# Optimization experiments

Measured on AMD Instinct MI355X. Metric: run time of the kernel, lower is better.

Reference implementation:

```python
import jax, jax.numpy as jnp
import numpy as np

N_NODES = 50000
N_EDGES = 800000
IN_CH = 512
HID = 128
OUT_CH = 2
N_GRAPHS = 64
EPS = 1e-5


def _gcn_conv(x, src, dst, W, b):
    # GCNConv: out = D^-1/2 (A + I) D^-1/2 (x W) + b  (PyG semantics, self-loops added)
    n = x.shape[0]
    h = x @ W  # [N, H]
    loop = jnp.arange(n)
    src2 = jnp.concatenate([src, loop])
    dst2 = jnp.concatenate([dst, loop])
    deg = jax.ops.segment_sum(jnp.ones_like(dst2, dtype=h.dtype), dst2, num_segments=n)
    dinv = jax.lax.rsqrt(deg)  # deg >= 1 due to self-loops
    norm = dinv[src2] * dinv[dst2]  # [E+N]
    msg = h[src2] * norm[:, None]  # gather + normalize
    out = jax.ops.segment_sum(msg, dst2, num_segments=n)  # scatter-add
    return out + b


def _batchnorm_eval(x, gamma, beta, rm, rv):
    return (x - rm) * jax.lax.rsqrt(rv + EPS) * gamma + beta


def setup_inputs() -> dict:
    key = jax.random.key(0)
    ks = jax.random.split(key, 16)
    x = jax.random.normal(ks[0], (N_NODES, IN_CH), dtype=jnp.float32)
    edge_index = jax.random.randint(ks[1], (2, N_EDGES), 0, N_NODES, dtype=jnp.int64)
    batch = jnp.sort(jax.random.randint(ks[2], (N_NODES,), 0, N_GRAPHS, dtype=jnp.int64))
    s1 = 1.0 / np.sqrt(IN_CH)
    s2 = 1.0 / np.sqrt(HID)
    return {
        'x': x,
        'edge_index': edge_index,
        'batch': batch,
        'W1': jax.random.normal(ks[3], (IN_CH, HID), dtype=jnp.float32) * s1,
        'b1': jnp.zeros((HID,), dtype=jnp.float32),
        'gamma1': jax.random.normal(ks[4], (HID,), dtype=jnp.float32) * 0.1 + 1.0,
        'beta1': jax.random.normal(ks[5], (HID,), dtype=jnp.float32) * 0.1,
        'rm1': jax.random.normal(ks[6], (HID,), dtype=jnp.float32) * 0.1,
        'rv1': jax.random.uniform(ks[7], (HID,), dtype=jnp.float32, minval=0.5, maxval=1.5),
        'W2': jax.random.normal(ks[8], (HID, HID), dtype=jnp.float32) * s2,
        'b2': jnp.zeros((HID,), dtype=jnp.float32),
        'gamma2': jax.random.normal(ks[9], (HID,), dtype=jnp.float32) * 0.1 + 1.0,
        'beta2': jax.random.normal(ks[10], (HID,), dtype=jnp.float32) * 0.1,
        'rm2': jax.random.normal(ks[11], (HID,), dtype=jnp.float32) * 0.1,
        'rv2': jax.random.uniform(ks[12], (HID,), dtype=jnp.float32, minval=0.5, maxval=1.5),
        'Wl': jax.random.normal(ks[13], (HID, OUT_CH), dtype=jnp.float32) * s2,
        'bl': jnp.zeros((OUT_CH,), dtype=jnp.float32),
    }


def reference(x, edge_index, batch, W1, b1, gamma1, beta1, rm1, rv1,
              W2, b2, gamma2, beta2, rm2, rv2, Wl, bl):
    # Eval mode: BatchNorm uses running stats; dropout is identity.
    src, dst = edge_index[0], edge_index[1]
    h = _gcn_conv(x, src, dst, W1, b1)
    h = jax.nn.relu(_batchnorm_eval(h, gamma1, beta1, rm1, rv1))
    h = _gcn_conv(h, src, dst, W2, b2)
    h = jax.nn.relu(_batchnorm_eval(h, gamma2, beta2, rm2, rv2))
    # global mean pool over graphs in the batch
    sums = jax.ops.segment_sum(h, batch, num_segments=N_GRAPHS)  # [G, H]
    counts = jax.ops.segment_sum(jnp.ones((h.shape[0],), dtype=h.dtype), batch, num_segments=N_GRAPHS)
    pooled = sums / jnp.maximum(counts, 1.0)[:, None]
    return pooled @ Wl + bl  # [G, OUT_CH]
```

## Files before the change

### kernel.cpp

```cpp
#include <hip/hip_runtime.h>

#define EPSV 1e-5f

typedef __attribute__((ext_vector_type(8))) short short8;
typedef __attribute__((ext_vector_type(4))) float f32x4;
typedef unsigned int uint;
typedef unsigned short ushort;

__global__ __launch_bounds__(256) void init_k(int* __restrict__ cnt,
                                              const int* __restrict__ batch,
                                              int* __restrict__ gstart,
                                              int nnodes, int ngraphs) {
    int i = blockIdx.x * 256 + threadIdx.x;
    if (i < nnodes) cnt[i] = 0;
    if (blockIdx.x == 0 && threadIdx.x <= ngraphs) {
        int g = threadIdx.x;
        int lo = 0, hi = nnodes;
        while (lo < hi) {
            int mid = (lo + hi) >> 1;
            if (batch[mid] < g) lo = mid + 1; else hi = mid;
        }
        gstart[g] = lo;
    }
}

__global__ __launch_bounds__(256) void degcount_k(const int* __restrict__ dst,
                                                  int* __restrict__ cnt,
                                                  int nedges) {
    int i = blockIdx.x * 256 + threadIdx.x;
    if (i < nedges) atomicAdd(&cnt[dst[i]], 1);
}

__global__ __launch_bounds__(256) void scan1_k(const int* __restrict__ cnt,
                                               int* __restrict__ rowptr,
                                               int* __restrict__ bsum,
                                               float* __restrict__ dinv, int n) {
    __shared__ int sh[256];
    const int tx = threadIdx.x;
    const int base = blockIdx.x * 1024;
    int v[4];
    int s = 0;
#pragma unroll
    for (int j = 0; j < 4; j++) {
        int idx = base + tx * 4 + j;
        v[j] = (idx < n) ? cnt[idx] : 0;
        if (idx < n) dinv[idx] = rsqrtf(1.0f + (float)v[j]);
        s += v[j];
    }
    sh[tx] = s;
    __syncthreads();
#pragma unroll
    for (int off = 1; off < 256; off <<= 1) {
        int t = (tx >= off) ? sh[tx - off] : 0;
        __syncthreads();
        sh[tx] += t;
        __syncthreads();
    }
    int run = sh[tx] - s;
#pragma unroll
    for (int j = 0; j < 4; j++) {
        int idx = base + tx * 4 + j;
        if (idx < n) rowptr[idx] = run;
        run += v[j];
    }
    if (tx == 255) bsum[blockIdx.x] = sh[255];
}

__global__ __launch_bounds__(64) void scan2_k(int* __restrict__ bsum, int nb) {
    __shared__ int sh[64];
    const int tx = threadIdx.x;
    int v = (tx < nb) ? bsum[tx] : 0;
    sh[tx] = v;
    __syncthreads();
#pragma unroll
    for (int off = 1; off < 64; off <<= 1) {
        int t = (tx >= off) ? sh[tx - off] : 0;
        __syncthreads();
        sh[tx] += t;
        __syncthreads();
    }
    if (tx < nb) bsum[tx] = sh[tx] - v;
}

__global__ __launch_bounds__(256) void scan3_k(int* __restrict__ rowptr,
                                               int* __restrict__ cur,
                                               const int* __restrict__ bsum,
                                               int n, int nedges) {
    const int tx = threadIdx.x;
    const int base = blockIdx.x * 1024;
    int off = bsum[blockIdx.x];
#pragma unroll
    for (int j = 0; j < 4; j++) {
        int idx = base + tx * 4 + j;
        if (idx < n) {
            int r = rowptr[idx] + off;
            rowptr[idx] = r;
            cur[idx] = r;
        }
    }
    if (blockIdx.x == 0 && tx == 0) rowptr[n] = nedges;
}

__global__ __launch_bounds__(256) void fill_k(const int* __restrict__ src,
                                              const int* __restrict__ dst,
                                              int* __restrict__ cur,
                                              int* __restrict__ esrc, int nedges) {
    int i = blockIdx.x * 256 + threadIdx.x;
    if (i >= nedges) return;
    int pos = atomicAdd(&cur[dst[i]], 1);
    esrc[pos] = src[i];
}

__global__ __launch_bounds__(256) void wprep_k(const float* __restrict__ W1,
                                               const float* __restrict__ W2,
                                               ushort* __restrict__ wt1,
                                               ushort* __restrict__ wt2) {
    int i = blockIdx.x * 256 + threadIdx.x;
    if (i < 512 * 128) {
        int k = i >> 7, c = i & 127;
        unsigned u = __builtin_bit_cast(unsigned, W1[i]);
        wt1[c * 512 + k] = (ushort)((u + 0x7fffu + ((u >> 16) & 1u)) >> 16);
    } else if (i < 512 * 128 + 128 * 128) {
        int j = i - 512 * 128;
        int k = j >> 7, c = j & 127;
        unsigned u = __builtin_bit_cast(unsigned, W2[j]);
        wt2[c * 128 + k] = (ushort)((u + 0x7fffu + ((u >> 16) & 1u)) >> 16);
    }
}

template <int K>
__global__ __launch_bounds__(256) void gemm_mfma_k(const float* __restrict__ X,
                                                   const ushort* __restrict__ wT,
                                                   const float* __restrict__ dinv,
                                                   float* __restrict__ H,
                                                   ushort* __restrict__ hb16,
                                                   int nrows) {
    __shared__ ushort bsm[2][8192];

    const int tx = threadIdx.x;
    const int wu = __builtin_amdgcn_readfirstlane(tx >> 6);
    const int l = tx & 63;
    const int lrow = l & 15;
    const int kgrp = l >> 4;
    const int wrow = wu >> 1;
    const int wcol = wu & 1;
    const int row0 = blockIdx.x * 32 + wrow * 16;

    const ushort* sp[4];
#pragma unroll
    for (int q = 0; q < 4; q++) {
        int chunk = (wu * 4 + q) * 64 + l;
        int c = chunk >> 3;
        int s = (chunk & 7) ^ (c & 7);
        sp[q] = wT + (size_t)c * K + s * 8;
    }

    int arow = row0 + lrow;
    if (arow >= nrows) arow = nrows - 1;
    const float* xrow = X + (size_t)arow * K + kgrp * 8;

    f32x4 acc[4];
#pragma unroll
    for (int g = 0; g < 4; g++) acc[g] = (f32x4){0.f, 0.f, 0.f, 0.f};

    auto STAGE = [&](int buf, int k0) {
#pragma unroll
        for (int q = 0; q < 4; q++) {
            const ushort* src = sp[q] + k0;
            ushort* dst = &bsm[buf][(wu * 4 + q) * 512];
            __builtin_amdgcn_global_load_lds(
                (const __attribute__((address_space(1))) unsigned int*)(const void*)src,
                (__attribute__((address_space(3))) unsigned int*)(void*)dst,
                16, 0, 0);
        }
    };

    constexpr int NIT = K / 64;

    STAGE(0, 0);
    asm volatile("" ::: "memory");
    f32x4 c0 = *reinterpret_cast<const f32x4*>(xrow);
    f32x4 c1 = *reinterpret_cast<const f32x4*>(xrow + 4);
    f32x4 c2 = *reinterpret_cast<const f32x4*>(xrow + 32);
    f32x4 c3 = *reinterpret_cast<const f32x4*>(xrow + 36);
    f32x4 d0 = c0, d1 = c1, d2 = c2, d3 = c3;
    if (NIT > 1) {
        d0 = *reinterpret_cast<const f32x4*>(xrow + 64);
        d1 = *reinterpret_cast<const f32x4*>(xrow + 68);
        d2 = *reinterpret_cast<const f32x4*>(xrow + 96);
        d3 = *reinterpret_cast<const f32x4*>(xrow + 100);
    }

#pragma unroll
    for (int i = 0; i < NIT; i++) {
        if (i == 0 && NIT > 1)   asm volatile("s_waitcnt vmcnt(8)" ::: "memory");
        else if (i + 1 < NIT)    asm volatile("s_waitcnt vmcnt(4)" ::: "memory");
        else                     asm volatile("s_waitcnt vmcnt(0)" ::: "memory");
        __builtin_amdgcn_s_barrier();
        __builtin_amdgcn_sched_barrier(0);

        if (i + 1 < NIT) STAGE((i + 1) & 1, (i + 1) * 64);
        asm volatile("" ::: "memory");

        f32x4 e0 = d0, e1 = d1, e2 = d2, e3 = d3;
        if (i + 2 < NIT) {
            const float* nx = xrow + (i + 2) * 64;
            e0 = *reinterpret_cast<const f32x4*>(nx);
            e1 = *reinterpret_cast<const f32x4*>(nx + 4);
            e2 = *reinterpret_cast<const f32x4*>(nx + 32);
            e3 = *reinterpret_cast<const f32x4*>(nx + 36);
        }

        const ushort* b = bsm[i & 1];
#pragma unroll
        for (int sub = 0; sub < 2; sub++) {
            short8 ah, al;
#pragma unroll
            for (int j = 0; j < 8; j++) {
                float f = (sub == 0) ? ((j < 4) ? c0[j] : c1[j - 4])
                                     : ((j < 4) ? c2[j] : c3[j - 4]);
                unsigned u = __builtin_bit_cast(unsigned, f);
                ah[j] = (short)(u >> 16);
                float hif = __builtin_bit_cast(float, u & 0xffff0000u);
                float lof = f - hif;
                al[j] = (short)(__builtin_bit_cast(unsigned, lof) >> 16);
            }
#pragma unroll
            for (int g = 0; g < 4; g++) {
                int cc = (wcol * 4 + g) * 16 + lrow;
                int phys = (sub * 4 + kgrp) ^ (cc & 7);
                short8 bb = *reinterpret_cast<const short8*>(&b[cc * 64 + phys * 8]);
                acc[g] = __builtin_amdgcn_mfma_f32_16x16x32_bf16(ah, bb, acc[g], 0, 0, 0);
                acc[g] = __builtin_amdgcn_mfma_f32_16x16x32_bf16(al, bb, acc[g], 0, 0, 0);
            }
        }

        c0 = d0; c1 = d1; c2 = d2; c3 = d3;
        d0 = e0; d1 = e1; d2 = e2; d3 = e3;
    }

#pragma unroll
    for (int r = 0; r < 4; r++) {
        int row = row0 + kgrp * 4 + r;
        if (row < nrows) {
            float dn = dinv[row];
            float* hrow = H + (size_t)row * 128 + wcol * 64 + lrow;
            ushort* hbrow = hb16 + (size_t)row * 128 + wcol * 64 + lrow;
#pragma unroll
            for (int g = 0; g < 4; g++) {
                float v = acc[g][r];
                hrow[g * 16] = v;
                unsigned u = __builtin_bit_cast(unsigned, v * dn);
                hbrow[g * 16] = (ushort)((u + 0x7fffu + ((u >> 16) & 1u)) >> 16);
            }
        }
    }
}

__global__ __launch_bounds__(256) void agg_k(const float* __restrict__ H,
                                             const uint* __restrict__ hb,
                                             const int* __restrict__ rowptr,
                                             const int* __restrict__ esrc,
                                             const float* __restrict__ dinv,
                                             const float* __restrict__ bias,
                                             const float* __restrict__ gamma,
                                             const float* __restrict__ beta,
                                             const float* __restrict__ rm,
                                             const float* __restrict__ rv,
                                             float* __restrict__ OUT,
                                             int nnodes) {
    int node = blockIdx.x * 4 + (threadIdx.x >> 6);
    if (node >= nnodes) return;
    node = __builtin_amdgcn_readfirstlane(node);
    const int l = threadIdx.x & 63;
    const int c = l * 2;
    const float dn = dinv[node];
    const int beg = rowptr[node], end = rowptr[node + 1];

    float2 hv = *reinterpret_cast<const float2*>(H + (size_t)node * 128 + c);
    float ax0 = hv.x * dn, ay0 = hv.y * dn;
    float ax1 = 0.f, ay1 = 0.f, ax2 = 0.f, ay2 = 0.f, ax3 = 0.f, ay3 = 0.f;
    const uint* hbl = hb + l;

    int j = beg;
    for (; j + 3 < end; j += 4) {
        int s0 = esrc[j], s1 = esrc[j + 1], s2 = esrc[j + 2], s3 = esrc[j + 3];
        uint u0 = hbl[(size_t)s0 * 64];
        uint u1 = hbl[(size_t)s1 * 64];
        uint u2 = hbl[(size_t)s2 * 64];
        uint u3 = hbl[(size_t)s3 * 64];
        ax0 += __builtin_bit_cast(float, u0 << 16);
        ay0 += __builtin_bit_cast(float, u0 & 0xffff0000u);
        ax1 += __builtin_bit_cast(float, u1 << 16);
        ay1 += __builtin_bit_cast(float, u1 & 0xffff0000u);
        ax2 += __builtin_bit_cast(float, u2 << 16);
        ay2 += __builtin_bit_cast(float, u2 & 0xffff0000u);
        ax3 += __builtin_bit_cast(float, u3 << 16);
        ay3 += __builtin_bit_cast(float, u3 & 0xffff0000u);
    }
    for (; j < end; j++) {
        uint u0 = hbl[(size_t)esrc[j] * 64];
        ax0 += __builtin_bit_cast(float, u0 << 16);
        ay0 += __builtin_bit_cast(float, u0 & 0xffff0000u);
    }
    float accx = (ax0 + ax1) + (ax2 + ax3);
    float accy = (ay0 + ay1) + (ay2 + ay3);

    float v0 = accx * dn + bias[c];
    float v1 = accy * dn + bias[c + 1];
    v0 = (v0 - rm[c])     * rsqrtf(rv[c] + EPSV)     * gamma[c]     + beta[c];
    v1 = (v1 - rm[c + 1]) * rsqrtf(rv[c + 1] + EPSV) * gamma[c + 1] + beta[c + 1];
    v0 = fmaxf(v0, 0.0f);
    v1 = fmaxf(v1, 0.0f);

    *reinterpret_cast<float2*>(OUT + (size_t)node * 128 + c) = make_float2(v0, v1);
}

__global__ __launch_bounds__(256) void pool1_k(const float* __restrict__ V,
                                               const int* __restrict__ gstart,
                                               float* __restrict__ partial) {
    __shared__ float sh[256];
    const int g = blockIdx.x >> 5;
    const int p = blockIdx.x & 31;
    const int tx = threadIdx.x;
    const int ch = tx & 127;
    const int sub = tx >> 7;
    const int beg = gstart[g], end = gstart[g + 1];
    const int chunk = (end - beg + 31) >> 5;
    const int s = beg + p * chunk;
    const int e = min(s + chunk, end);
    float acc = 0.0f;
    for (int i = s + sub; i < e; i += 2)
        acc += V[(size_t)i * 128 + ch];
    sh[tx] = acc;
    __syncthreads();
    if (tx < 128)
        partial[(size_t)blockIdx.x * 128 + tx] = sh[tx] + sh[tx + 128];
}

__global__ __launch_bounds__(128) void pool2_k(const float* __restrict__ partial,
                                               const int* __restrict__ gstart,
                                               float* __restrict__ pooled) {
    const int g = blockIdx.x;
    const int ch = threadIdx.x;
    float s = 0.0f;
#pragma unroll
    for (int p = 0; p < 32; p++)
        s += partial[(size_t)((g << 5) + p) * 128 + ch];
    float cnt = fmaxf((float)(gstart[g + 1] - gstart[g]), 1.0f);
    pooled[g * 128 + ch] = s / cnt;
}

__global__ __launch_bounds__(128) void final_k(const float* __restrict__ pooled,
                                               const float* __restrict__ Wl,
                                               const float* __restrict__ bl,
                                               float* __restrict__ out) {
    int tx = threadIdx.x;
    int g = tx >> 1, o = tx & 1;
    float s = 0.0f;
#pragma unroll 8
    for (int c = 0; c < 128; c++) s += pooled[g * 128 + c] * Wl[c * 2 + o];
    out[tx] = s + bl[o];
}

extern "C" void kernel_launch(void* const* d_in, const int* in_sizes, int n_in,
                              void* d_out, int out_size, void* d_ws, size_t ws_size,
                              hipStream_t stream) {
    const float* x      = (const float*)d_in[0];
    const int*   ei     = (const int*)d_in[1];
    const int*   batch  = (const int*)d_in[2];
    const float* W1     = (const float*)d_in[3];
    const float* b1     = (const float*)d_in[4];
    const float* gamma1 = (const float*)d_in[5];
    const float* beta1  = (const float*)d_in[6];
    const float* rm1    = (const float*)d_in[7];
    const float* rv1    = (const float*)d_in[8];
    const float* W2     = (const float*)d_in[9];
    const float* b2     = (const float*)d_in[10];
    const float* gamma2 = (const float*)d_in[11];
    const float* beta2  = (const float*)d_in[12];
    const float* rm2    = (const float*)d_in[13];
    const float* rv2    = (const float*)d_in[14];
    const float* Wl     = (const float*)d_in[15];
    const float* bl     = (const float*)d_in[16];
    float* out = (float*)d_out;

    const int nnodes  = in_sizes[2];
    const int nedges  = in_sizes[1] / 2;
    const int ngraphs = 64;
    const int* srcp = ei;
    const int* dstp = ei + nedges;

    float* wsA     = (float*)d_ws;
    float* wsB     = wsA + (size_t)nnodes * 128;
    float* dinv    = wsB + (size_t)nnodes * 128;
    float* pooled  = dinv + nnodes;
    float* partial = pooled + 64 * 128;
    int*   cnt     = (int*)(partial + 64 * 32 * 128);
    int*   rowptr  = cnt + nnodes;
    int*   cur     = rowptr + nnodes + 1;
    int*   bsum    = cur + nnodes;
    int*   gstart  = bsum + 64;
    int*   esrc    = gstart + 65;
    uintptr_t wp   = ((uintptr_t)(esrc + nedges) + 15) & ~(uintptr_t)15;
    ushort* wt1  = (ushort*)wp;
    ushort* wt2  = wt1 + 512 * 128;
    ushort* hb16 = wt2 + 128 * 128;
    uint*   hb   = (uint*)hb16;

    dim3 blk(256);
    const int gNodes = (nnodes + 255) / 256;
    const int gEdges = (nedges + 255) / 256;
    const int gGemm  = (nnodes + 31) / 32;
    const int gAgg   = (nnodes + 3) / 4;
    const int nScanB = (nnodes + 1023) / 1024;

    init_k<<<gNodes, blk, 0, stream>>>(cnt, batch, gstart, nnodes, ngraphs);
    wprep_k<<<(512 * 128 + 128 * 128 + 255) / 256, blk, 0, stream>>>(W1, W2, wt1, wt2);
    degcount_k<<<gEdges, blk, 0, stream>>>(dstp, cnt, nedges);
    scan1_k<<<nScanB, blk, 0, stream>>>(cnt, rowptr, bsum, dinv, nnodes);
    scan2_k<<<1, 64, 0, stream>>>(bsum, nScanB);
    scan3_k<<<nScanB, blk, 0, stream>>>(rowptr, cur, bsum, nnodes, nedges);
    fill_k<<<gEdges, blk, 0, stream>>>(srcp, dstp, cur, esrc, nedges);

    gemm_mfma_k<512><<<gGemm, blk, 0, stream>>>(x, wt1, dinv, wsA, hb16, nnodes);
    agg_k<<<gAgg, blk, 0, stream>>>(wsA, hb, rowptr, esrc, dinv, b1, gamma1, beta1,
                                    rm1, rv1, wsB, nnodes);

    gemm_mfma_k<128><<<gGemm, blk, 0, stream>>>(wsB, wt2, dinv, wsA, hb16, nnodes);
    agg_k<<<gAgg, blk, 0, stream>>>(wsA, hb, rowptr, esrc, dinv, b2, gamma2, beta2,
                                    rm2, rv2, wsB, nnodes);

    pool1_k<<<ngraphs * 32, blk, 0, stream>>>(wsB, gstart, partial);
    pool2_k<<<ngraphs, 128, 0, stream>>>(partial, gstart, pooled);
    final_k<<<1, 128, 0, stream>>>(pooled, Wl, bl, out);
}
```

Before: 263.8 us.

## Stage full weight matrix in LDS once per block and double rows per block

The GEMM kernel now loads the entire transposed bf16 weight matrix into shared memory once at block start, instead of double-buffering 64-wide K slices with per-iteration barriers and waitcnts. Blocks grow to 512 threads covering 64 rows, which halves the grid and the total weight traffic from L2. In exchange, shared-memory use reaches 128KB for K=512, limiting each CU to roughly one block. The weight load also no longer overlaps with the MFMA work.

```diff
diff --git a/kernel.cpp b/kernel.cpp
--- a/kernel.cpp
+++ b/kernel.cpp
@@ -129,13 +129,13 @@
 }
 
 template <int K>
-__global__ __launch_bounds__(256) void gemm_mfma_k(const float* __restrict__ X,
+__global__ __launch_bounds__(512) void gemm_mfma_k(const float* __restrict__ X,
                                                    const ushort* __restrict__ wT,
                                                    const float* __restrict__ dinv,
                                                    float* __restrict__ H,
                                                    ushort* __restrict__ hb16,
                                                    int nrows) {
-    __shared__ ushort bsm[2][8192];
+    __shared__ ushort wsm[128 * K];
 
     const int tx = threadIdx.x;
     const int wu = __builtin_amdgcn_readfirstlane(tx >> 6);
@@ -144,15 +144,21 @@
     const int kgrp = l >> 4;
     const int wrow = wu >> 1;
     const int wcol = wu & 1;
-    const int row0 = blockIdx.x * 32 + wrow * 16;
-
-    const ushort* sp[4];
-#pragma unroll
-    for (int q = 0; q < 4; q++) {
-        int chunk = (wu * 4 + q) * 64 + l;
-        int c = chunk >> 3;
-        int s = (chunk & 7) ^ (c & 7);
-        sp[q] = wT + (size_t)c * K + s * 8;
+    const int row0 = blockIdx.x * 64 + wrow * 16;
+
+    constexpr int NPW = K / 32;
+#pragma unroll
+    for (int q = 0; q < NPW; q++) {
+        int j = wu * NPW + q;
+        int byte0 = j * 1024 + l * 16;
+        int c = byte0 / (K * 2);
+        int slot = (byte0 % (K * 2)) >> 4;
+        const ushort* src = wT + (size_t)c * K + ((slot ^ (c & 7)) * 8);
+        ushort* dst = &wsm[j * 512];
+        __builtin_amdgcn_global_load_lds(
+            (const __attribute__((address_space(1))) unsigned int*)(const void*)src,
+            (__attribute__((address_space(3))) unsigned int*)(void*)dst,
+            16, 0, 0);
     }
 
     int arow = row0 + lrow;
@@ -163,22 +169,8 @@
 #pragma unroll
     for (int g = 0; g < 4; g++) acc[g] = (f32x4){0.f, 0.f, 0.f, 0.f};
 
-    auto STAGE = [&](int buf, int k0) {
-#pragma unroll
-        for (int q = 0; q < 4; q++) {
-            const ushort* src = sp[q] + k0;
-            ushort* dst = &bsm[buf][(wu * 4 + q) * 512];
-            __builtin_amdgcn_global_load_lds(
-                (const __attribute__((address_space(1))) unsigned int*)(const void*)src,
-                (__attribute__((address_space(3))) unsigned int*)(void*)dst,
-                16, 0, 0);
-        }
-    };
-
     constexpr int NIT = K / 64;
 
-    STAGE(0, 0);
-    asm volatile("" ::: "memory");
     f32x4 c0 = *reinterpret_cast<const f32x4*>(xrow);
     f32x4 c1 = *reinterpret_cast<const f32x4*>(xrow + 4);
     f32x4 c2 = *reinterpret_cast<const f32x4*>(xrow + 32);
@@ -191,17 +183,10 @@
         d3 = *reinterpret_cast<const f32x4*>(xrow + 100);
     }
 
+    __syncthreads();
+
 #pragma unroll
     for (int i = 0; i < NIT; i++) {
-        if (i == 0 && NIT > 1)   asm volatile("s_waitcnt vmcnt(8)" ::: "memory");
-        else if (i + 1 < NIT)    asm volatile("s_waitcnt vmcnt(4)" ::: "memory");
-        else                     asm volatile("s_waitcnt vmcnt(0)" ::: "memory");
-        __builtin_amdgcn_s_barrier();
-        __builtin_amdgcn_sched_barrier(0);
-
-        if (i + 1 < NIT) STAGE((i + 1) & 1, (i + 1) * 64);
-        asm volatile("" ::: "memory");
-
         f32x4 e0 = d0, e1 = d1, e2 = d2, e3 = d3;
         if (i + 2 < NIT) {
             const float* nx = xrow + (i + 2) * 64;
@@ -211,7 +196,6 @@
             e3 = *reinterpret_cast<const f32x4*>(nx + 36);
         }
 
-        const ushort* b = bsm[i & 1];
 #pragma unroll
         for (int sub = 0; sub < 2; sub++) {
             short8 ah, al;
@@ -225,11 +209,13 @@
                 float lof = f - hif;
                 al[j] = (short)(__builtin_bit_cast(unsigned, lof) >> 16);
             }
+            int slot = i * 8 + sub * 4 + kgrp;
 #pragma unroll
             for (int g = 0; g < 4; g++) {
                 int cc = (wcol * 4 + g) * 16 + lrow;
-                int phys = (sub * 4 + kgrp) ^ (cc & 7);
-                short8 bb = *reinterpret_cast<const short8*>(&b[cc * 64 + phys * 8]);
+                int phys = slot ^ (cc & 7);
+                short8 bb = *reinterpret_cast<const short8*>(
+                    &wsm[(size_t)cc * K + phys * 8]);
                 acc[g] = __builtin_amdgcn_mfma_f32_16x16x32_bf16(ah, bb, acc[g], 0, 0, 0);
                 acc[g] = __builtin_amdgcn_mfma_f32_16x16x32_bf16(al, bb, acc[g], 0, 0, 0);
             }
@@ -411,7 +397,7 @@
     dim3 blk(256);
     const int gNodes = (nnodes + 255) / 256;
     const int gEdges = (nedges + 255) / 256;
-    const int gGemm  = (nnodes + 31) / 32;
+    const int gGemm  = (nnodes + 63) / 64;
     const int gAgg   = (nnodes + 3) / 4;
     const int nScanB = (nnodes + 1023) / 1024;
 
@@ -423,11 +409,11 @@
     scan3_k<<<nScanB, blk, 0, stream>>>(rowptr, cur, bsum, nnodes, nedges);
     fill_k<<<gEdges, blk, 0, stream>>>(srcp, dstp, cur, esrc, nedges);
 
-    gemm_mfma_k<512><<<gGemm, blk, 0, stream>>>(x, wt1, dinv, wsA, hb16, nnodes);
+    gemm_mfma_k<512><<<gGemm, dim3(512), 0, stream>>>(x, wt1, dinv, wsA, hb16, nnodes);
     agg_k<<<gAgg, blk, 0, stream>>>(wsA, hb, rowptr, esrc, dinv, b1, gamma1, beta1,
                                     rm1, rv1, wsB, nnodes);
 
-    gemm_mfma_k<128><<<gGemm, blk, 0, stream>>>(wsB, wt2, dinv, wsA, hb16, nnodes);
+    gemm_mfma_k<128><<<gGemm, dim3(512), 0, stream>>>(wsB, wt2, dinv, wsA, hb16, nnodes);
     agg_k<<<gAgg, blk, 0, stream>>>(wsA, hb, rowptr, esrc, dinv, b2, gamma2, beta2,
                                     rm2, rv2, wsB, nnodes);
 
```

Measured after the change: 275.6 us. 1.04x slower.

## Stage X tiles through LDS and widen GEMM tile to 64 rows by 128 columns

Applied to the files above, without the earlier changes.

The GEMM now loads X tiles asynchronously into swizzled LDS with global_load_lds instead of prefetching them into registers. Each wave computes a 16x128 output strip (8 accumulators) instead of 16x64, so a block covers 64 rows and W is reused across twice as many rows. The aim is to halve the number of times W tiles are reloaded and to stream the fp32 activations more efficiently. In exchange, LDS use grows to about 64KB per block, which can limit occupancy, and the loop now waits with vmcnt(0) each iteration, dropping the finer-grained prefetch overlap.

```diff
diff --git a/kernel.cpp b/kernel.cpp
--- a/kernel.cpp
+++ b/kernel.cpp
@@ -135,90 +135,76 @@
                                                    float* __restrict__ H,
                                                    ushort* __restrict__ hb16,
                                                    int nrows) {
-    __shared__ ushort bsm[2][8192];
+    __shared__ float  lAs[2][64 * 64];
+    __shared__ ushort lBs[2][128 * 64];
 
     const int tx = threadIdx.x;
     const int wu = __builtin_amdgcn_readfirstlane(tx >> 6);
     const int l = tx & 63;
     const int lrow = l & 15;
     const int kgrp = l >> 4;
-    const int wrow = wu >> 1;
-    const int wcol = wu & 1;
-    const int row0 = blockIdx.x * 32 + wrow * 16;
-
-    const ushort* sp[4];
-#pragma unroll
-    for (int q = 0; q < 4; q++) {
-        int chunk = (wu * 4 + q) * 64 + l;
-        int c = chunk >> 3;
-        int s = (chunk & 7) ^ (c & 7);
-        sp[q] = wT + (size_t)c * K + s * 8;
-    }
-
-    int arow = row0 + lrow;
-    if (arow >= nrows) arow = nrows - 1;
-    const float* xrow = X + (size_t)arow * K + kgrp * 8;
-
-    f32x4 acc[4];
-#pragma unroll
-    for (int g = 0; g < 4; g++) acc[g] = (f32x4){0.f, 0.f, 0.f, 0.f};
+    const int rowB = blockIdx.x * 64;
+    const int row0 = rowB + wu * 16;
+
+    f32x4 acc[8];
+#pragma unroll
+    for (int g = 0; g < 8; g++) acc[g] = (f32x4){0.f, 0.f, 0.f, 0.f};
 
     auto STAGE = [&](int buf, int k0) {
 #pragma unroll
         for (int q = 0; q < 4; q++) {
-            const ushort* src = sp[q] + k0;
-            ushort* dst = &bsm[buf][(wu * 4 + q) * 512];
+            int j = wu * 4 + q;
+            int row = j * 4 + (l >> 4);
+            int slot = l & 15;
+            int grow = rowB + row;
+            if (grow >= nrows) grow = nrows - 1;
+            const float* src = X + (size_t)grow * K + k0 + ((slot ^ (row & 15)) * 4);
+            float* dst = &lAs[buf][j * 256];
             __builtin_amdgcn_global_load_lds(
                 (const __attribute__((address_space(1))) unsigned int*)(const void*)src,
                 (__attribute__((address_space(3))) unsigned int*)(void*)dst,
                 16, 0, 0);
         }
+#pragma unroll
+        for (int q = 0; q < 4; q++) {
+            int j = wu * 4 + q;
+            int col = j * 8 + (l >> 3);
+            int slot = l & 7;
+            const ushort* src = wT + (size_t)col * K + k0 + ((slot ^ (col & 7)) * 8);
+            ushort* dst = &lBs[buf][j * 512];
+            __builtin_amdgcn_global_load_lds(
+                (const __attribute__((address_space(1))) unsigned int*)(const void*)src,
+                (__attribute__((address_space(3))) unsigned int*)(void*)dst,
+                16, 0, 0);
+        }
     };
 
     constexpr int NIT = K / 64;
 
     STAGE(0, 0);
-    asm volatile("" ::: "memory");
-    f32x4 c0 = *reinterpret_cast<const f32x4*>(xrow);
-    f32x4 c1 = *reinterpret_cast<const f32x4*>(xrow + 4);
-    f32x4 c2 = *reinterpret_cast<const f32x4*>(xrow + 32);
-    f32x4 c3 = *reinterpret_cast<const f32x4*>(xrow + 36);
-    f32x4 d0 = c0, d1 = c1, d2 = c2, d3 = c3;
-    if (NIT > 1) {
-        d0 = *reinterpret_cast<const f32x4*>(xrow + 64);
-        d1 = *reinterpret_cast<const f32x4*>(xrow + 68);
-        d2 = *reinterpret_cast<const f32x4*>(xrow + 96);
-        d3 = *reinterpret_cast<const f32x4*>(xrow + 100);
-    }
 
 #pragma unroll
     for (int i = 0; i < NIT; i++) {
-        if (i == 0 && NIT > 1)   asm volatile("s_waitcnt vmcnt(8)" ::: "memory");
-        else if (i + 1 < NIT)    asm volatile("s_waitcnt vmcnt(4)" ::: "memory");
-        else                     asm volatile("s_waitcnt vmcnt(0)" ::: "memory");
+        asm volatile("s_waitcnt vmcnt(0)" ::: "memory");
         __builtin_amdgcn_s_barrier();
         __builtin_amdgcn_sched_barrier(0);
 
         if (i + 1 < NIT) STAGE((i + 1) & 1, (i + 1) * 64);
         asm volatile("" ::: "memory");
 
-        f32x4 e0 = d0, e1 = d1, e2 = d2, e3 = d3;
-        if (i + 2 < NIT) {
-            const float* nx = xrow + (i + 2) * 64;
-            e0 = *reinterpret_cast<const f32x4*>(nx);
-            e1 = *reinterpret_cast<const f32x4*>(nx + 4);
-            e2 = *reinterpret_cast<const f32x4*>(nx + 32);
-            e3 = *reinterpret_cast<const f32x4*>(nx + 36);
-        }
-
-        const ushort* b = bsm[i & 1];
-#pragma unroll
-        for (int sub = 0; sub < 2; sub++) {
+        const int buf = i & 1;
+        const int trow = wu * 16 + lrow;
+#pragma unroll
+        for (int ks = 0; ks < 2; ks++) {
+            int s16 = (ks * 4 + kgrp) * 2;
+            f32x4 a0 = *reinterpret_cast<const f32x4*>(
+                &lAs[buf][trow * 64 + ((s16 ^ lrow) & 15) * 4]);
+            f32x4 a1 = *reinterpret_cast<const f32x4*>(
+                &lAs[buf][trow * 64 + (((s16 + 1) ^ lrow) & 15) * 4]);
             short8 ah, al;
 #pragma unroll
             for (int j = 0; j < 8; j++) {
-                float f = (sub == 0) ? ((j < 4) ? c0[j] : c1[j - 4])
-                                     : ((j < 4) ? c2[j] : c3[j - 4]);
+                float f = (j < 4) ? a0[j] : a1[j - 4];
                 unsigned u = __builtin_bit_cast(unsigned, f);
                 ah[j] = (short)(u >> 16);
                 float hif = __builtin_bit_cast(float, u & 0xffff0000u);
@@ -226,17 +212,15 @@
                 al[j] = (short)(__builtin_bit_cast(unsigned, lof) >> 16);
             }
 #pragma unroll
-            for (int g = 0; g < 4; g++) {
-                int cc = (wcol * 4 + g) * 16 + lrow;
-                int phys = (sub * 4 + kgrp) ^ (cc & 7);
-                short8 bb = *reinterpret_cast<const short8*>(&b[cc * 64 + phys * 8]);
+            for (int g = 0; g < 8; g++) {
+                int cc = g * 16 + lrow;
+                int phys = (ks * 4 + kgrp) ^ (cc & 7);
+                short8 bb = *reinterpret_cast<const short8*>(
+                    &lBs[buf][cc * 64 + phys * 8]);
                 acc[g] = __builtin_amdgcn_mfma_f32_16x16x32_bf16(ah, bb, acc[g], 0, 0, 0);
                 acc[g] = __builtin_amdgcn_mfma_f32_16x16x32_bf16(al, bb, acc[g], 0, 0, 0);
             }
         }
-
-        c0 = d0; c1 = d1; c2 = d2; c3 = d3;
-        d0 = e0; d1 = e1; d2 = e2; d3 = e3;
     }
 
 #pragma unroll
@@ -244,10 +228,10 @@
         int row = row0 + kgrp * 4 + r;
         if (row < nrows) {
             float dn = dinv[row];
-            float* hrow = H + (size_t)row * 128 + wcol * 64 + lrow;
-            ushort* hbrow = hb16 + (size_t)row * 128 + wcol * 64 + lrow;
-#pragma unroll
-            for (int g = 0; g < 4; g++) {
+            float* hrow = H + (size_t)row * 128 + lrow;
+            ushort* hbrow = hb16 + (size_t)row * 128 + lrow;
+#pragma unroll
+            for (int g = 0; g < 8; g++) {
                 float v = acc[g][r];
                 hrow[g * 16] = v;
                 unsigned u = __builtin_bit_cast(unsigned, v * dn);
@@ -411,7 +395,7 @@
     dim3 blk(256);
     const int gNodes = (nnodes + 255) / 256;
     const int gEdges = (nedges + 255) / 256;
-    const int gGemm  = (nnodes + 31) / 32;
+    const int gGemm  = (nnodes + 63) / 64;
     const int gAgg   = (nnodes + 3) / 4;
     const int nScanB = (nnodes + 1023) / 1024;
 
```

Measured after the change: 258.5 us. 2.0% less time.
